# Optimization experiments

Hardware: AMD Instinct MI355X
Metric: run time of the kernel (lower is better)

## Reference

```python
import jax, jax.numpy as jnp
import numpy as np

# dims: N batch, C in-channels, T frames, V joints, H heads, HD per-head dim, O out-channels
N, C, T, V = 32, 64, 256, 25
H, HD, O = 8, 8, 64  # HD = max(C//8, 8)
SCALE = HD ** -0.5
EPS = 1e-5


def setup_inputs() -> dict:
    key = jax.random.key(0)
    ks = jax.random.split(key, 10)
    return {
        "x": jax.random.normal(ks[0], (N, C, T, V), jnp.float32),
        "ln_gamma": jnp.ones((C,), jnp.float32),
        "ln_beta": jnp.zeros((C,), jnp.float32),
        "w_qk": jax.random.normal(ks[1], (C, 2 * H * HD), jnp.float32),  # to_qk init N(0,1)
        "b_qk": jax.random.normal(ks[2], (2 * H * HD,), jnp.float32) * 0.02,
        "shared_topology": jax.random.uniform(ks[3], (H, V, V), jnp.float32),
        "conv_w": jax.random.normal(ks[4], (H, O, C), jnp.float32) * np.sqrt(2.0 / (O * H)),
        "conv_b": jnp.zeros((H, O), jnp.float32),
        "bn_gamma": jnp.full((O,), 1e-6, jnp.float32),
        "bn_beta": jnp.zeros((O,), jnp.float32),
        "bn_mean": jnp.zeros((O,), jnp.float32),
        "bn_var": jnp.ones((O,), jnp.float32),
    }


def reference(x, ln_gamma, ln_beta, w_qk, b_qk, shared_topology,
              conv_w, conv_b, bn_gamma, bn_beta, bn_mean, bn_var):
    # ---- SelfAttention over joints ----
    y = jnp.transpose(x, (0, 2, 3, 1))                 # [N,T,V,C]
    mu = jnp.mean(y, axis=-1, keepdims=True)
    var = jnp.var(y, axis=-1, keepdims=True)
    yn = (y - mu) * jax.lax.rsqrt(var + EPS) * ln_gamma + ln_beta
    qk = yn @ w_qk + b_qk                              # [N,T,V,2*H*HD]
    B = N * T
    q, k = jnp.split(qk.reshape(B, V, 2 * H * HD), 2, axis=-1)
    q = q.reshape(B, V, H, HD).transpose(0, 2, 1, 3)   # [B,H,V,HD]
    k = k.reshape(B, V, H, HD).transpose(0, 2, 1, 3)
    dots = jnp.einsum("bhid,bhjd->bhij", q, k) * SCALE
    attn = jax.nn.softmax(dots, axis=-1).astype(jnp.float32)  # [B,H,V,V]

    # ---- attention-gated graph conv ----
    A = attn * shared_topology[None]                   # [B,H,V,V]
    feat = jnp.transpose(x, (0, 2, 3, 1)).reshape(B, V, C)  # [B,V,C]
    z = jnp.einsum("bhuv,bvc->bhuc", A, feat)          # per-head aggregate [B,H,V,C]
    # fused per-head 1x1 convs + sum over heads
    out = jnp.einsum("bhuc,hoc->buo", z, conv_w) + conv_b.sum(0)  # [B,V,O]
    out = out.reshape(N, T, V, O).transpose(0, 3, 1, 2)           # [N,O,T,V]

    # ---- BatchNorm (inference-mode) + residual + ReLU ----
    g = (bn_gamma * jax.lax.rsqrt(bn_var + EPS))[None, :, None, None]
    b = (bn_beta - bn_mean * bn_gamma * jax.lax.rsqrt(bn_var + EPS))[None, :, None, None]
    out = out * g + b
    out = jax.nn.relu(out + x)  # down is identity (in_c == out_c)
    return out
```

## Files before the change

### kernel.cpp

```cpp
#include <hip/hip_runtime.h>
#include <math.h>

#define SCALE_L2E 0.51006972157f
#define EPSV 1e-5f

typedef __attribute__((ext_vector_type(8))) short bf16x8;
typedef __attribute__((ext_vector_type(4))) float f32x4;
typedef __attribute__((ext_vector_type(16))) float f32x16;
typedef __attribute__((ext_vector_type(4))) int i32x4;
typedef __attribute__((ext_vector_type(2))) int i32x2;

static __device__ __forceinline__ unsigned short bfh(float f) {
    return (unsigned short)(__builtin_bit_cast(unsigned int, f) >> 16);
}
static __device__ __forceinline__ int pack2(float lo, float hi) {
    return __builtin_amdgcn_perm(__builtin_bit_cast(unsigned int, hi),
                                 __builtin_bit_cast(unsigned int, lo), 0x07060302u);
}
#define LGKM0() __asm__ __volatile__("s_waitcnt lgkmcnt(0)" ::: "memory")

__global__ void prep_kernel(const float* __restrict__ w_qk,
                            const float* __restrict__ conv_w,
                            const float* __restrict__ conv_b,
                            const float* __restrict__ bn_g, const float* __restrict__ bn_b,
                            const float* __restrict__ bn_m, const float* __restrict__ bn_v,
                            unsigned short* __restrict__ ws) {
    int i = blockIdx.x * 256 + threadIdx.x;
    if (i < 8192) {
        int f = i >> 9, rem = i & 511, l = rem >> 3, j = rem & 7;
        int nt = f >> 1, ks = f & 1;
        int k = ks * 32 + (l >> 4) * 8 + j;
        int nn = nt * 16 + (l & 15);
        ws[i] = bfh(w_qk[k * 128 + nn]);
    } else if (i < 40960) {
        int i2 = i - 8192;
        int g = i2 >> 9, rem = i2 & 511, l = rem >> 3, j = rem & 7;
        int h = g >> 3, nt = (g >> 1) & 3, ks = g & 1;
        int c = ks * 32 + (l >> 4) * 8 + j;
        int o = nt * 16 + (l & 15);
        ws[i] = bfh(conv_w[h * 4096 + o * 64 + c]);
    } else if (i < 41024) {
        int o = i - 40960;
        float gv = bn_g[o] * rsqrtf(bn_v[o] + EPSV);
        float bb = bn_b[o] - bn_m[o] * gv;
        float cb = 0.f;
        for (int h = 0; h < 8; h++) cb += conv_b[h * 64 + o];
        float* wsf = (float*)(ws + 40960);
        wsf[o] = gv;
        wsf[64 + o] = bb + cb * gv;
    }
}

__global__ __launch_bounds__(256, 2)
void sagc_kernel(const float* __restrict__ x,
                 const float* __restrict__ ln_g, const float* __restrict__ ln_b,
                 const float* __restrict__ b_qk,
                 const float* __restrict__ topo,
                 const unsigned short* __restrict__ ws,
                 float* __restrict__ out)
{
    __shared__ __align__(16) unsigned char smem[36864];
    const int tid = threadIdx.x;
    const int lane = tid & 63, wv = tid >> 6;
    const int l15 = lane & 15, quad = lane >> 4;
    const int r32 = lane & 31, hi = lane >> 5;

    unsigned char* my = smem + wv * 9216;
    unsigned short* qbuf = (unsigned short*)my;
    unsigned short* kbuf = (unsigned short*)(my + 1536);
    unsigned char*  fwb  = my;
    unsigned char*  pb0  = my + 4096;
    unsigned char*  pb1  = my + 4096 + 2560;

    const unsigned short* wqk = ws;
    const unsigned short* w2f = ws + 8192;
    const float* bnA = (const float*)(ws + 40960);
    const float* bnB = bnA + 64;

    const int tile = blockIdx.x * 4 + wv;
    const int n = tile >> 8, t = tile & 255;
    const float* xg = x + (size_t)n * 409600 + (size_t)t * 25;
    float* og = out + (size_t)n * 409600 + (size_t)t * 25;

    float xf[2][2][8];
    #pragma unroll
    for (int mt = 0; mt < 2; mt++) {
        const int v = mt * 16 + l15;
        const bool ok = (v < 25);
        const float* xc = xg + v;
        #pragma unroll
        for (int ks = 0; ks < 2; ks++)
            #pragma unroll
            for (int j = 0; j < 8; j++) {
                int c = ks * 32 + quad * 8 + j;
                xf[mt][ks][j] = ok ? xc[c * 6400] : 0.f;
            }
    }

    bf16x8 xa[2][2];
    float sum_[2] = {0.f, 0.f}, ssq_[2] = {0.f, 0.f};
    #pragma unroll
    for (int mt = 0; mt < 2; mt++)
        #pragma unroll
        for (int ks = 0; ks < 2; ks++) {
            i32x4 pa;
            #pragma unroll
            for (int q = 0; q < 4; q++)
                pa[q] = pack2(xf[mt][ks][2 * q], xf[mt][ks][2 * q + 1]);
            xa[mt][ks] = __builtin_bit_cast(bf16x8, pa);
            #pragma unroll
            for (int j = 0; j < 8; j++) {
                float a = xf[mt][ks][j];
                sum_[mt] += a;
                ssq_[mt] += a * a;
            }
        }

    float muv[2], rsv[2];
    #pragma unroll
    for (int mt = 0; mt < 2; mt++) {
        sum_[mt] += __shfl_xor(sum_[mt], 16);
        sum_[mt] += __shfl_xor(sum_[mt], 32);
        ssq_[mt] += __shfl_xor(ssq_[mt], 16);
        ssq_[mt] += __shfl_xor(ssq_[mt], 32);
        muv[mt] = sum_[mt] * 0.015625f;
        rsv[mt] = rsqrtf(ssq_[mt] * 0.015625f - muv[mt] * muv[mt] + EPSV);
    }

    bf16x8 yna[2][2];
    #pragma unroll
    for (int ks = 0; ks < 2; ks++) {
        f32x4 ga = *(const f32x4*)&ln_g[ks * 32 + quad * 8];
        f32x4 gb = *(const f32x4*)&ln_g[ks * 32 + quad * 8 + 4];
        f32x4 ba = *(const f32x4*)&ln_b[ks * 32 + quad * 8];
        f32x4 bb = *(const f32x4*)&ln_b[ks * 32 + quad * 8 + 4];
        #pragma unroll
        for (int mt = 0; mt < 2; mt++) {
            float yv[8];
            #pragma unroll
            for (int j = 0; j < 8; j++) {
                float g = (j < 4) ? ga[j] : gb[j - 4];
                float bt = (j < 4) ? ba[j] : bb[j - 4];
                yv[j] = (xf[mt][ks][j] - muv[mt]) * rsv[mt] * g + bt;
            }
            i32x4 p;
            #pragma unroll
            for (int q = 0; q < 4; q++) p[q] = pack2(yv[2 * q], yv[2 * q + 1]);
            yna[mt][ks] = __builtin_bit_cast(bf16x8, p);
        }
    }

    f32x4 acc[2][4];
    #pragma unroll
    for (int mt = 0; mt < 2; mt++)
        #pragma unroll
        for (int nt = 0; nt < 4; nt++)
            acc[mt][nt] = (f32x4){0.f, 0.f, 0.f, 0.f};

    const f32x4 z4 = {0.f, 0.f, 0.f, 0.f};
    const bf16x8 z8 = {0, 0, 0, 0, 0, 0, 0, 0};

    const int sw4 = (l15 >> 2) & 3;
    unsigned char* w0p = fwb + ((((quad >> 1) ^ sw4)) << 4) + (quad & 1) * 8;
    unsigned char* w1p = fwb + (((((quad >> 1) ^ sw4)) ^ 2) << 4) + (quad & 1) * 8;
    unsigned char* brp = fwb + l15 * 64 + ((quad ^ sw4) << 4);

    const int uc = (r32 < 25) ? r32 : 24;

    auto softmax_store = [&](f32x16& dd, const float* tp, unsigned char* Pb) {
        dd[12] = hi ? -3e30f : dd[12];
        dd[13] = -3e30f; dd[14] = -3e30f; dd[15] = -3e30f;
        float t8[8];
        #pragma unroll
        for (int r = 0; r < 8; r++) t8[r] = fmaxf(dd[r], dd[r + 8]);
        #pragma unroll
        for (int r = 0; r < 4; r++) t8[r] = fmaxf(t8[r], t8[r + 4]);
        float m = fmaxf(fmaxf(t8[0], t8[1]), fmaxf(t8[2], t8[3]));
        m = fmaxf(m, __shfl_xor(m, 32));
        float s0 = 0.f, s1 = 0.f, s2 = 0.f, s3 = 0.f;
        #pragma unroll
        for (int r = 0; r < 16; r += 4) {
            dd[r]     = __builtin_amdgcn_exp2f(dd[r] - m);     s0 += dd[r];
            dd[r + 1] = __builtin_amdgcn_exp2f(dd[r + 1] - m); s1 += dd[r + 1];
            dd[r + 2] = __builtin_amdgcn_exp2f(dd[r + 2] - m); s2 += dd[r + 2];
            dd[r + 3] = __builtin_amdgcn_exp2f(dd[r + 3] - m); s3 += dd[r + 3];
        }
        float s = (s0 + s1) + (s2 + s3);
        s += __shfl_xor(s, 32);
        float inv = __builtin_amdgcn_rcpf(s);
        #pragma unroll
        for (int r = 0; r < 16; r++) dd[r] = dd[r] * inv * tp[r];
        if (r32 < 25) {
            unsigned char* rowp = Pb + r32 * 80 + hi * 8;
            *(i32x2*)(rowp +  0) = (i32x2){pack2(dd[0], dd[1]),   pack2(dd[2], dd[3])};
            *(i32x2*)(rowp + 16) = (i32x2){pack2(dd[4], dd[5]),   pack2(dd[6], dd[7])};
            *(i32x2*)(rowp + 32) = (i32x2){pack2(dd[8], dd[9]),   pack2(dd[10], dd[11])};
            *(i32x2*)(rowp + 48) = (i32x2){pack2(dd[12], dd[13]), pack2(dd[14], dd[15])};
        }
    };

    const f32x16 z16 = {0.f,0.f,0.f,0.f,0.f,0.f,0.f,0.f,0.f,0.f,0.f,0.f,0.f,0.f,0.f,0.f};

    #pragma unroll
    for (int hp = 0; hp < 4; hp++) {
        #pragma unroll
        for (int tsel = 0; tsel < 2; tsel++) {
            int nt = tsel ? (4 + hp) : hp;
            bf16x8 b0 = *(const bf16x8*)&wqk[(nt * 2 + 0) * 512 + lane * 8];
            bf16x8 b1 = *(const bf16x8*)&wqk[(nt * 2 + 1) * 512 + lane * 8];
            float bias = b_qk[(tsel ? 64 : 0) + hp * 16 + l15];
            unsigned short* buf = tsel ? kbuf : qbuf;
            #pragma unroll
            for (int mt = 0; mt < 2; mt++) {
                f32x4 d = __builtin_amdgcn_mfma_f32_16x16x32_bf16(yna[mt][0], b0, z4, 0, 0, 0);
                d = __builtin_amdgcn_mfma_f32_16x16x32_bf16(yna[mt][1], b1, d, 0, 0, 0);
                #pragma unroll
                for (int r = 0; r < 4; r++) {
                    int u = mt * 16 + quad * 4 + r;
                    if (u < 25) {
                        float val = d[r] + bias;
                        if (!tsel) val *= SCALE_L2E;
                        buf[u * 24 + l15] = bfh(val);
                    }
                }
            }
        }

        float tp0[16];
        {
            const float* tb = topo + (hp * 2 + 0) * 625 + uc * 25 + hi * 4;
            #pragma unroll
            for (int r = 0; r < 16; r++) {
                int off = (r < 12) ? ((r & 3) + (r >> 2) * 8)
                        : (r == 12 ? (hi ? 0 : 24) : 0);
                tp0[r] = tb[off];
            }
        }
        LGKM0();

        f32x16 p0;
        {
            bf16x8 ak = z8, bq = z8;
            if (hi == 0) {
                ak = *(const bf16x8*)&kbuf[r32 * 24 + 0];
                bq = *(const bf16x8*)&qbuf[r32 * 24 + 0];
            }
            p0 = __builtin_amdgcn_mfma_f32_32x32x16_bf16(ak, bq, z16, 0, 0, 0);
        }
        float tp1[16];
        {
            const float* tb = topo + (hp * 2 + 1) * 625 + uc * 25 + hi * 4;
            #pragma unroll
            for (int r = 0; r < 16; r++) {
                int off = (r < 12) ? ((r & 3) + (r >> 2) * 8)
                        : (r == 12 ? (hi ? 0 : 24) : 0);
                tp1[r] = tb[off];
            }
        }
        f32x16 p1;
        {
            bf16x8 ak = z8, bq = z8;
            if (hi == 0) {
                ak = *(const bf16x8*)&kbuf[r32 * 24 + 8];
                bq = *(const bf16x8*)&qbuf[r32 * 24 + 8];
            }
            p1 = __builtin_amdgcn_mfma_f32_32x32x16_bf16(ak, bq, z16, 0, 0, 0);
        }

        softmax_store(p0, tp0, pb0);
        softmax_store(p1, tp1, pb1);

        bf16x8 w2e[8];
        #pragma unroll
        for (int nt = 0; nt < 4; nt++) {
            int h = hp * 2;
            w2e[2 * nt]     = *(const bf16x8*)&w2f[((h * 4 + nt) * 2 + 0) * 512 + lane * 8];
            w2e[2 * nt + 1] = *(const bf16x8*)&w2f[((h * 4 + nt) * 2 + 1) * 512 + lane * 8];
        }

        #pragma unroll
        for (int nt = 0; nt < 4; nt++) {
            f32x4 dw0 = __builtin_amdgcn_mfma_f32_16x16x32_bf16(xa[0][0], w2e[2 * nt], z4, 0, 0, 0);
            dw0 = __builtin_amdgcn_mfma_f32_16x16x32_bf16(xa[0][1], w2e[2 * nt + 1], dw0, 0, 0, 0);
            f32x4 dw1 = __builtin_amdgcn_mfma_f32_16x16x32_bf16(xa[1][0], w2e[2 * nt], z4, 0, 0, 0);
            dw1 = __builtin_amdgcn_mfma_f32_16x16x32_bf16(xa[1][1], w2e[2 * nt + 1], dw1, 0, 0, 0);
            i32x2 q0 = {pack2(dw0[0], dw0[1]), pack2(dw0[2], dw0[3])};
            i32x2 q1 = {pack2(dw1[0], dw1[1]), pack2(dw1[2], dw1[3])};
            *(i32x2*)(w0p + nt * 1024 + l15 * 64) = q0;
            *(i32x2*)(w1p + nt * 1024 + l15 * 64) = q1;
        }
        bf16x8 w2o[8];
        #pragma unroll
        for (int nt = 0; nt < 4; nt++) {
            int h = hp * 2 + 1;
            w2o[2 * nt]     = *(const bf16x8*)&w2f[((h * 4 + nt) * 2 + 0) * 512 + lane * 8];
            w2o[2 * nt + 1] = *(const bf16x8*)&w2f[((h * 4 + nt) * 2 + 1) * 512 + lane * 8];
        }
        LGKM0();

        {
            bf16x8 ag0 = *(const bf16x8*)(pb0 + l15 * 80 + quad * 16);
            bf16x8 ag1 = *(const bf16x8*)(pb0 + (16 + l15) * 80 + quad * 16);
            #pragma unroll
            for (int nt = 0; nt < 4; nt++) {
                bf16x8 br = *(const bf16x8*)(brp + nt * 1024);
                acc[0][nt] = __builtin_amdgcn_mfma_f32_16x16x32_bf16(ag0, br, acc[0][nt], 0, 0, 0);
                acc[1][nt] = __builtin_amdgcn_mfma_f32_16x16x32_bf16(ag1, br, acc[1][nt], 0, 0, 0);
            }
        }

        #pragma unroll
        for (int nt = 0; nt < 4; nt++) {
            f32x4 dw0 = __builtin_amdgcn_mfma_f32_16x16x32_bf16(xa[0][0], w2o[2 * nt], z4, 0, 0, 0);
            dw0 = __builtin_amdgcn_mfma_f32_16x16x32_bf16(xa[0][1], w2o[2 * nt + 1], dw0, 0, 0, 0);
            f32x4 dw1 = __builtin_amdgcn_mfma_f32_16x16x32_bf16(xa[1][0], w2o[2 * nt], z4, 0, 0, 0);
            dw1 = __builtin_amdgcn_mfma_f32_16x16x32_bf16(xa[1][1], w2o[2 * nt + 1], dw1, 0, 0, 0);
            i32x2 q0 = {pack2(dw0[0], dw0[1]), pack2(dw0[2], dw0[3])};
            i32x2 q1 = {pack2(dw1[0], dw1[1]), pack2(dw1[2], dw1[3])};
            *(i32x2*)(w0p + nt * 1024 + l15 * 64) = q0;
            *(i32x2*)(w1p + nt * 1024 + l15 * 64) = q1;
        }
        LGKM0();

        {
            bf16x8 ag0 = *(const bf16x8*)(pb1 + l15 * 80 + quad * 16);
            bf16x8 ag1 = *(const bf16x8*)(pb1 + (16 + l15) * 80 + quad * 16);
            #pragma unroll
            for (int nt = 0; nt < 4; nt++) {
                bf16x8 br = *(const bf16x8*)(brp + nt * 1024);
                acc[0][nt] = __builtin_amdgcn_mfma_f32_16x16x32_bf16(ag0, br, acc[0][nt], 0, 0, 0);
                acc[1][nt] = __builtin_amdgcn_mfma_f32_16x16x32_bf16(ag1, br, acc[1][nt], 0, 0, 0);
            }
        }
    }

    #pragma unroll
    for (int nt = 0; nt < 4; nt++) {
        int o = nt * 16 + l15;
        float gA = bnA[o], gB = bnB[o];
        #pragma unroll
        for (int mt = 0; mt < 2; mt++) {
            int ub = mt * 16 + quad * 4;
            #pragma unroll
            for (int r = 0; r < 4; r++) {
                int u = ub + r;
                if (u < 25) {
                    float val = acc[mt][nt][r] * gA + gB + xg[o * 6400 + u];
                    og[o * 6400 + u] = fmaxf(val, 0.f);
                }
            }
        }
    }
}

extern "C" void kernel_launch(void* const* d_in, const int* in_sizes, int n_in,
                              void* d_out, int out_size, void* d_ws, size_t ws_size,
                              hipStream_t stream) {
    const float* x      = (const float*)d_in[0];
    const float* ln_g   = (const float*)d_in[1];
    const float* ln_b   = (const float*)d_in[2];
    const float* w_qk   = (const float*)d_in[3];
    const float* b_qk   = (const float*)d_in[4];
    const float* topo   = (const float*)d_in[5];
    const float* conv_w = (const float*)d_in[6];
    const float* conv_b = (const float*)d_in[7];
    const float* bn_g   = (const float*)d_in[8];
    const float* bn_b   = (const float*)d_in[9];
    const float* bn_m   = (const float*)d_in[10];
    const float* bn_v   = (const float*)d_in[11];
    float* outp = (float*)d_out;
    unsigned short* wsp = (unsigned short*)d_ws;

    hipLaunchKernelGGL(prep_kernel, dim3(161), dim3(256), 0, stream,
                       w_qk, conv_w, conv_b, bn_g, bn_b, bn_m, bn_v, wsp);
    hipLaunchKernelGGL(sagc_kernel, dim3(2048), dim3(256), 0, stream,
                       x, ln_g, ln_b, b_qk, topo, (const unsigned short*)wsp, outp);
}
```

Baseline: 188.8 us.

## Process two time-frame tiles per wavefront to reuse weight and topology loads

Each wave now handles two adjacent (n,t) tiles instead of one, with the grid halved and per-wave shared memory doubled. Weight fragments (w_qk, conv_w) and topology gathers are loaded once per head and used for both tiles, and the independent MFMA chains of the two tiles are interleaved to hide latency. In exchange, register pressure roughly doubles, launch bounds drop to one block per SIMD group, and LDS use doubles, which lowers occupancy.

```diff
diff --git a/kernel.cpp b/kernel.cpp
--- a/kernel.cpp
+++ b/kernel.cpp
@@ -18,6 +18,7 @@
                                  __builtin_bit_cast(unsigned int, lo), 0x07060302u);
 }
 #define LGKM0() __asm__ __volatile__("s_waitcnt lgkmcnt(0)" ::: "memory")
+#define MFMA16(a, b, c) __builtin_amdgcn_mfma_f32_16x16x32_bf16((a), (b), (c), 0, 0, 0)
 
 __global__ void prep_kernel(const float* __restrict__ w_qk,
                             const float* __restrict__ conv_w,
@@ -51,7 +52,7 @@
     }
 }
 
-__global__ __launch_bounds__(256, 2)
+__global__ __launch_bounds__(256, 1)
 void sagc_kernel(const float* __restrict__ x,
                  const float* __restrict__ ln_g, const float* __restrict__ ln_b,
                  const float* __restrict__ b_qk,
@@ -59,13 +60,13 @@
                  const unsigned short* __restrict__ ws,
                  float* __restrict__ out)
 {
-    __shared__ __align__(16) unsigned char smem[36864];
+    __shared__ __align__(16) unsigned char smem[73728];
     const int tid = threadIdx.x;
     const int lane = tid & 63, wv = tid >> 6;
     const int l15 = lane & 15, quad = lane >> 4;
     const int r32 = lane & 31, hi = lane >> 5;
 
-    unsigned char* my = smem + wv * 9216;
+    unsigned char* my = smem + wv * 18432;
     unsigned short* qbuf = (unsigned short*)my;
     unsigned short* kbuf = (unsigned short*)(my + 1536);
     unsigned char*  fwb  = my;
@@ -77,88 +78,94 @@
     const float* bnA = (const float*)(ws + 40960);
     const float* bnB = bnA + 64;
 
-    const int tile = blockIdx.x * 4 + wv;
-    const int n = tile >> 8, t = tile & 255;
-    const float* xg = x + (size_t)n * 409600 + (size_t)t * 25;
-    float* og = out + (size_t)n * 409600 + (size_t)t * 25;
-
-    float xf[2][2][8];
-    #pragma unroll
-    for (int mt = 0; mt < 2; mt++) {
-        const int v = mt * 16 + l15;
-        const bool ok = (v < 25);
-        const float* xc = xg + v;
-        #pragma unroll
-        for (int ks = 0; ks < 2; ks++)
-            #pragma unroll
-            for (int j = 0; j < 8; j++) {
-                int c = ks * 32 + quad * 8 + j;
-                xf[mt][ks][j] = ok ? xc[c * 6400] : 0.f;
+    const int tileA = (blockIdx.x * 4 + wv) * 2;
+    const int n = tileA >> 8, tA = tileA & 255;
+    const float* xgA = x + (size_t)n * 409600 + (size_t)tA * 25;
+    const float* xgB = xgA + 25;
+    float* ogA = out + (size_t)n * 409600 + (size_t)tA * 25;
+    float* ogB = ogA + 25;
+
+    auto prologue = [&](const float* xg, bf16x8 (&xa)[2][2], bf16x8 (&yna)[2][2]) {
+        float xf[2][2][8];
+        #pragma unroll
+        for (int mt = 0; mt < 2; mt++) {
+            const int v = mt * 16 + l15;
+            const bool ok = (v < 25);
+            const float* xc = xg + v;
+            #pragma unroll
+            for (int ks = 0; ks < 2; ks++)
+                #pragma unroll
+                for (int j = 0; j < 8; j++) {
+                    int c = ks * 32 + quad * 8 + j;
+                    xf[mt][ks][j] = ok ? xc[c * 6400] : 0.f;
+                }
+        }
+        float sum_[2] = {0.f, 0.f}, ssq_[2] = {0.f, 0.f};
+        #pragma unroll
+        for (int mt = 0; mt < 2; mt++)
+            #pragma unroll
+            for (int ks = 0; ks < 2; ks++) {
+                i32x4 pa;
+                #pragma unroll
+                for (int q = 0; q < 4; q++)
+                    pa[q] = pack2(xf[mt][ks][2 * q], xf[mt][ks][2 * q + 1]);
+                xa[mt][ks] = __builtin_bit_cast(bf16x8, pa);
+                #pragma unroll
+                for (int j = 0; j < 8; j++) {
+                    float a = xf[mt][ks][j];
+                    sum_[mt] += a;
+                    ssq_[mt] += a * a;
+                }
             }
-    }
-
-    bf16x8 xa[2][2];
-    float sum_[2] = {0.f, 0.f}, ssq_[2] = {0.f, 0.f};
+        float muv[2], rsv[2];
+        #pragma unroll
+        for (int mt = 0; mt < 2; mt++) {
+            sum_[mt] += __shfl_xor(sum_[mt], 16);
+            sum_[mt] += __shfl_xor(sum_[mt], 32);
+            ssq_[mt] += __shfl_xor(ssq_[mt], 16);
+            ssq_[mt] += __shfl_xor(ssq_[mt], 32);
+            muv[mt] = sum_[mt] * 0.015625f;
+            rsv[mt] = rsqrtf(ssq_[mt] * 0.015625f - muv[mt] * muv[mt] + EPSV);
+        }
+        #pragma unroll
+        for (int ks = 0; ks < 2; ks++) {
+            f32x4 ga = *(const f32x4*)&ln_g[ks * 32 + quad * 8];
+            f32x4 gb = *(const f32x4*)&ln_g[ks * 32 + quad * 8 + 4];
+            f32x4 ba = *(const f32x4*)&ln_b[ks * 32 + quad * 8];
+            f32x4 bb = *(const f32x4*)&ln_b[ks * 32 + quad * 8 + 4];
+            #pragma unroll
+            for (int mt = 0; mt < 2; mt++) {
+                float yv[8];
+                #pragma unroll
+                for (int j = 0; j < 8; j++) {
+                    float g = (j < 4) ? ga[j] : gb[j - 4];
+                    float bt = (j < 4) ? ba[j] : bb[j - 4];
+                    yv[j] = (xf[mt][ks][j] - muv[mt]) * rsv[mt] * g + bt;
+                }
+                i32x4 p;
+                #pragma unroll
+                for (int q = 0; q < 4; q++) p[q] = pack2(yv[2 * q], yv[2 * q + 1]);
+                yna[mt][ks] = __builtin_bit_cast(bf16x8, p);
+            }
+        }
+    };
+
+    bf16x8 xaA[2][2], ynaA[2][2], xaB[2][2], ynaB[2][2];
+    prologue(xgA, xaA, ynaA);
+    prologue(xgB, xaB, ynaB);
+
+    f32x4 accA[2][4], accB[2][4];
     #pragma unroll
     for (int mt = 0; mt < 2; mt++)
         #pragma unroll
-        for (int ks = 0; ks < 2; ks++) {
-            i32x4 pa;
-            #pragma unroll
-            for (int q = 0; q < 4; q++)
-                pa[q] = pack2(xf[mt][ks][2 * q], xf[mt][ks][2 * q + 1]);
-            xa[mt][ks] = __builtin_bit_cast(bf16x8, pa);
-            #pragma unroll
-            for (int j = 0; j < 8; j++) {
-                float a = xf[mt][ks][j];
-                sum_[mt] += a;
-                ssq_[mt] += a * a;
-            }
-        }
-
-    float muv[2], rsv[2];
-    #pragma unroll
-    for (int mt = 0; mt < 2; mt++) {
-        sum_[mt] += __shfl_xor(sum_[mt], 16);
-        sum_[mt] += __shfl_xor(sum_[mt], 32);
-        ssq_[mt] += __shfl_xor(ssq_[mt], 16);
-        ssq_[mt] += __shfl_xor(ssq_[mt], 32);
-        muv[mt] = sum_[mt] * 0.015625f;
-        rsv[mt] = rsqrtf(ssq_[mt] * 0.015625f - muv[mt] * muv[mt] + EPSV);
-    }
-
-    bf16x8 yna[2][2];
-    #pragma unroll
-    for (int ks = 0; ks < 2; ks++) {
-        f32x4 ga = *(const f32x4*)&ln_g[ks * 32 + quad * 8];
-        f32x4 gb = *(const f32x4*)&ln_g[ks * 32 + quad * 8 + 4];
-        f32x4 ba = *(const f32x4*)&ln_b[ks * 32 + quad * 8];
-        f32x4 bb = *(const f32x4*)&ln_b[ks * 32 + quad * 8 + 4];
-        #pragma unroll
-        for (int mt = 0; mt < 2; mt++) {
-            float yv[8];
-            #pragma unroll
-            for (int j = 0; j < 8; j++) {
-                float g = (j < 4) ? ga[j] : gb[j - 4];
-                float bt = (j < 4) ? ba[j] : bb[j - 4];
-                yv[j] = (xf[mt][ks][j] - muv[mt]) * rsv[mt] * g + bt;
-            }
-            i32x4 p;
-            #pragma unroll
-            for (int q = 0; q < 4; q++) p[q] = pack2(yv[2 * q], yv[2 * q + 1]);
-            yna[mt][ks] = __builtin_bit_cast(bf16x8, p);
-        }
-    }
-
-    f32x4 acc[2][4];
-    #pragma unroll
-    for (int mt = 0; mt < 2; mt++)
-        #pragma unroll
-        for (int nt = 0; nt < 4; nt++)
-            acc[mt][nt] = (f32x4){0.f, 0.f, 0.f, 0.f};
+        for (int nt = 0; nt < 4; nt++) {
+            accA[mt][nt] = (f32x4){0.f, 0.f, 0.f, 0.f};
+            accB[mt][nt] = (f32x4){0.f, 0.f, 0.f, 0.f};
+        }
 
     const f32x4 z4 = {0.f, 0.f, 0.f, 0.f};
     const bf16x8 z8 = {0, 0, 0, 0, 0, 0, 0, 0};
+    const f32x16 z16 = {0.f,0.f,0.f,0.f,0.f,0.f,0.f,0.f,0.f,0.f,0.f,0.f,0.f,0.f,0.f,0.f};
 
     const int sw4 = (l15 >> 2) & 3;
     unsigned char* w0p = fwb + ((((quad >> 1) ^ sw4)) << 4) + (quad & 1) * 8;
@@ -199,9 +206,50 @@
         }
     };
 
-    const f32x16 z16 = {0.f,0.f,0.f,0.f,0.f,0.f,0.f,0.f,0.f,0.f,0.f,0.f,0.f,0.f,0.f,0.f};
-
-    #pragma unroll
+    auto topo_gather = [&](int h, float (&tp)[16]) {
+        const float* tb = topo + h * 625 + uc * 25 + hi * 4;
+        #pragma unroll
+        for (int r = 0; r < 16; r++) {
+            int off = (r < 12) ? ((r & 3) + (r >> 2) * 8)
+                    : (r == 12 ? (hi ? 0 : 24) : 0);
+            tp[r] = tb[off];
+        }
+    };
+
+    auto dots = [&](int tdoff, int hh) -> f32x16 {
+        bf16x8 ak = z8, bq = z8;
+        if (hi == 0) {
+            ak = *(const bf16x8*)((unsigned char*)kbuf + tdoff + r32 * 48 + hh * 16);
+            bq = *(const bf16x8*)((unsigned char*)qbuf + tdoff + r32 * 48 + hh * 16);
+        }
+        return __builtin_amdgcn_mfma_f32_32x32x16_bf16(ak, bq, z16, 0, 0, 0);
+    };
+
+    auto fw_phase = [&](bf16x8 (&xa)[2][2], const bf16x8* w2, int tdoff) {
+        #pragma unroll
+        for (int nt = 0; nt < 4; nt++) {
+            f32x4 dw0 = MFMA16(xa[0][0], w2[2 * nt], z4);
+            dw0 = MFMA16(xa[0][1], w2[2 * nt + 1], dw0);
+            f32x4 dw1 = MFMA16(xa[1][0], w2[2 * nt], z4);
+            dw1 = MFMA16(xa[1][1], w2[2 * nt + 1], dw1);
+            i32x2 q0 = {pack2(dw0[0], dw0[1]), pack2(dw0[2], dw0[3])};
+            i32x2 q1 = {pack2(dw1[0], dw1[1]), pack2(dw1[2], dw1[3])};
+            *(i32x2*)(w0p + tdoff + nt * 1024 + l15 * 64) = q0;
+            *(i32x2*)(w1p + tdoff + nt * 1024 + l15 * 64) = q1;
+        }
+    };
+
+    auto pv_phase = [&](f32x4 (&acc)[2][4], unsigned char* Pb, int tdoff) {
+        bf16x8 ag0 = *(const bf16x8*)(Pb + tdoff + l15 * 80 + quad * 16);
+        bf16x8 ag1 = *(const bf16x8*)(Pb + tdoff + 1280 + l15 * 80 + quad * 16);
+        #pragma unroll
+        for (int nt = 0; nt < 4; nt++) {
+            bf16x8 br = *(const bf16x8*)(brp + tdoff + nt * 1024);
+            acc[0][nt] = MFMA16(ag0, br, acc[0][nt]);
+            acc[1][nt] = MFMA16(ag1, br, acc[1][nt]);
+        }
+    };
+
     for (int hp = 0; hp < 4; hp++) {
         #pragma unroll
         for (int tsel = 0; tsel < 2; tsel++) {
@@ -209,66 +257,45 @@
             bf16x8 b0 = *(const bf16x8*)&wqk[(nt * 2 + 0) * 512 + lane * 8];
             bf16x8 b1 = *(const bf16x8*)&wqk[(nt * 2 + 1) * 512 + lane * 8];
             float bias = b_qk[(tsel ? 64 : 0) + hp * 16 + l15];
-            unsigned short* buf = tsel ? kbuf : qbuf;
-            #pragma unroll
-            for (int mt = 0; mt < 2; mt++) {
-                f32x4 d = __builtin_amdgcn_mfma_f32_16x16x32_bf16(yna[mt][0], b0, z4, 0, 0, 0);
-                d = __builtin_amdgcn_mfma_f32_16x16x32_bf16(yna[mt][1], b1, d, 0, 0, 0);
-                #pragma unroll
-                for (int r = 0; r < 4; r++) {
-                    int u = mt * 16 + quad * 4 + r;
-                    if (u < 25) {
-                        float val = d[r] + bias;
-                        if (!tsel) val *= SCALE_L2E;
-                        buf[u * 24 + l15] = bfh(val);
+            #pragma unroll
+            for (int td = 0; td < 2; td++) {
+                unsigned short* buf = (unsigned short*)((unsigned char*)(tsel ? kbuf : qbuf) + td * 9216);
+                #pragma unroll
+                for (int mt = 0; mt < 2; mt++) {
+                    const bf16x8* yn = td ? ynaB[mt] : ynaA[mt];
+                    f32x4 d = MFMA16(yn[0], b0, z4);
+                    d = MFMA16(yn[1], b1, d);
+                    #pragma unroll
+                    for (int r = 0; r < 4; r++) {
+                        int u = mt * 16 + quad * 4 + r;
+                        if (u < 25) {
+                            float val = d[r] + bias;
+                            if (!tsel) val *= SCALE_L2E;
+                            buf[u * 24 + l15] = bfh(val);
+                        }
                     }
                 }
             }
         }
 
         float tp0[16];
+        topo_gather(hp * 2, tp0);
+        LGKM0();
+
         {
-            const float* tb = topo + (hp * 2 + 0) * 625 + uc * 25 + hi * 4;
-            #pragma unroll
-            for (int r = 0; r < 16; r++) {
-                int off = (r < 12) ? ((r & 3) + (r >> 2) * 8)
-                        : (r == 12 ? (hi ? 0 : 24) : 0);
-                tp0[r] = tb[off];
-            }
-        }
-        LGKM0();
-
-        f32x16 p0;
+            f32x16 pA = dots(0, 0);
+            f32x16 pB = dots(9216, 0);
+            softmax_store(pA, tp0, pb0);
+            softmax_store(pB, tp0, pb0 + 9216);
+        }
+        float tp1[16];
+        topo_gather(hp * 2 + 1, tp1);
         {
-            bf16x8 ak = z8, bq = z8;
-            if (hi == 0) {
-                ak = *(const bf16x8*)&kbuf[r32 * 24 + 0];
-                bq = *(const bf16x8*)&qbuf[r32 * 24 + 0];
-            }
-            p0 = __builtin_amdgcn_mfma_f32_32x32x16_bf16(ak, bq, z16, 0, 0, 0);
-        }
-        float tp1[16];
-        {
-            const float* tb = topo + (hp * 2 + 1) * 625 + uc * 25 + hi * 4;
-            #pragma unroll
-            for (int r = 0; r < 16; r++) {
-                int off = (r < 12) ? ((r & 3) + (r >> 2) * 8)
-                        : (r == 12 ? (hi ? 0 : 24) : 0);
-                tp1[r] = tb[off];
-            }
-        }
-        f32x16 p1;
-        {
-            bf16x8 ak = z8, bq = z8;
-            if (hi == 0) {
-                ak = *(const bf16x8*)&kbuf[r32 * 24 + 8];
-                bq = *(const bf16x8*)&qbuf[r32 * 24 + 8];
-            }
-            p1 = __builtin_amdgcn_mfma_f32_32x32x16_bf16(ak, bq, z16, 0, 0, 0);
-        }
-
-        softmax_store(p0, tp0, pb0);
-        softmax_store(p1, tp1, pb1);
+            f32x16 pA = dots(0, 1);
+            f32x16 pB = dots(9216, 1);
+            softmax_store(pA, tp1, pb1);
+            softmax_store(pB, tp1, pb1 + 9216);
+        }
 
         bf16x8 w2e[8];
         #pragma unroll
@@ -277,18 +304,8 @@
             w2e[2 * nt]     = *(const bf16x8*)&w2f[((h * 4 + nt) * 2 + 0) * 512 + lane * 8];
             w2e[2 * nt + 1] = *(const bf16x8*)&w2f[((h * 4 + nt) * 2 + 1) * 512 + lane * 8];
         }
-
-        #pragma unroll
-        for (int nt = 0; nt < 4; nt++) {
-            f32x4 dw0 = __builtin_amdgcn_mfma_f32_16x16x32_bf16(xa[0][0], w2e[2 * nt], z4, 0, 0, 0);
-            dw0 = __builtin_amdgcn_mfma_f32_16x16x32_bf16(xa[0][1], w2e[2 * nt + 1], dw0, 0, 0, 0);
-            f32x4 dw1 = __builtin_amdgcn_mfma_f32_16x16x32_bf16(xa[1][0], w2e[2 * nt], z4, 0, 0, 0);
-            dw1 = __builtin_amdgcn_mfma_f32_16x16x32_bf16(xa[1][1], w2e[2 * nt + 1], dw1, 0, 0, 0);
-            i32x2 q0 = {pack2(dw0[0], dw0[1]), pack2(dw0[2], dw0[3])};
-            i32x2 q1 = {pack2(dw1[0], dw1[1]), pack2(dw1[2], dw1[3])};
-            *(i32x2*)(w0p + nt * 1024 + l15 * 64) = q0;
-            *(i32x2*)(w1p + nt * 1024 + l15 * 64) = q1;
-        }
+        fw_phase(xaA, w2e, 0);
+        fw_phase(xaB, w2e, 9216);
         bf16x8 w2o[8];
         #pragma unroll
         for (int nt = 0; nt < 4; nt++) {
@@ -298,59 +315,38 @@
         }
         LGKM0();
 
-        {
-            bf16x8 ag0 = *(const bf16x8*)(pb0 + l15 * 80 + quad * 16);
-            bf16x8 ag1 = *(const bf16x8*)(pb0 + (16 + l15) * 80 + quad * 16);
-            #pragma unroll
-            for (int nt = 0; nt < 4; nt++) {
-                bf16x8 br = *(const bf16x8*)(brp + nt * 1024);
-                acc[0][nt] = __builtin_amdgcn_mfma_f32_16x16x32_bf16(ag0, br, acc[0][nt], 0, 0, 0);
-                acc[1][nt] = __builtin_amdgcn_mfma_f32_16x16x32_bf16(ag1, br, acc[1][nt], 0, 0, 0);
+        pv_phase(accA, pb0, 0);
+        pv_phase(accB, pb0, 9216);
+
+        fw_phase(xaA, w2o, 0);
+        fw_phase(xaB, w2o, 9216);
+        LGKM0();
+
+        pv_phase(accA, pb1, 0);
+        pv_phase(accB, pb1, 9216);
+    }
+
+    auto epilogue = [&](f32x4 (&acc)[2][4], const float* xg, float* og) {
+        #pragma unroll
+        for (int nt = 0; nt < 4; nt++) {
+            int o = nt * 16 + l15;
+            float gA = bnA[o], gB = bnB[o];
+            #pragma unroll
+            for (int mt = 0; mt < 2; mt++) {
+                int ub = mt * 16 + quad * 4;
+                #pragma unroll
+                for (int r = 0; r < 4; r++) {
+                    int u = ub + r;
+                    if (u < 25) {
+                        float val = acc[mt][nt][r] * gA + gB + xg[o * 6400 + u];
+                        og[o * 6400 + u] = fmaxf(val, 0.f);
+                    }
+                }
             }
         }
-
-        #pragma unroll
-        for (int nt = 0; nt < 4; nt++) {
-            f32x4 dw0 = __builtin_amdgcn_mfma_f32_16x16x32_bf16(xa[0][0], w2o[2 * nt], z4, 0, 0, 0);
-            dw0 = __builtin_amdgcn_mfma_f32_16x16x32_bf16(xa[0][1], w2o[2 * nt + 1], dw0, 0, 0, 0);
-            f32x4 dw1 = __builtin_amdgcn_mfma_f32_16x16x32_bf16(xa[1][0], w2o[2 * nt], z4, 0, 0, 0);
-            dw1 = __builtin_amdgcn_mfma_f32_16x16x32_bf16(xa[1][1], w2o[2 * nt + 1], dw1, 0, 0, 0);
-            i32x2 q0 = {pack2(dw0[0], dw0[1]), pack2(dw0[2], dw0[3])};
-            i32x2 q1 = {pack2(dw1[0], dw1[1]), pack2(dw1[2], dw1[3])};
-            *(i32x2*)(w0p + nt * 1024 + l15 * 64) = q0;
-            *(i32x2*)(w1p + nt * 1024 + l15 * 64) = q1;
-        }
-        LGKM0();
-
-        {
-            bf16x8 ag0 = *(const bf16x8*)(pb1 + l15 * 80 + quad * 16);
-            bf16x8 ag1 = *(const bf16x8*)(pb1 + (16 + l15) * 80 + quad * 16);
-            #pragma unroll
-            for (int nt = 0; nt < 4; nt++) {
-                bf16x8 br = *(const bf16x8*)(brp + nt * 1024);
-                acc[0][nt] = __builtin_amdgcn_mfma_f32_16x16x32_bf16(ag0, br, acc[0][nt], 0, 0, 0);
-                acc[1][nt] = __builtin_amdgcn_mfma_f32_16x16x32_bf16(ag1, br, acc[1][nt], 0, 0, 0);
-            }
-        }
-    }
-
-    #pragma unroll
-    for (int nt = 0; nt < 4; nt++) {
-        int o = nt * 16 + l15;
-        float gA = bnA[o], gB = bnB[o];
-        #pragma unroll
-        for (int mt = 0; mt < 2; mt++) {
-            int ub = mt * 16 + quad * 4;
-            #pragma unroll
-            for (int r = 0; r < 4; r++) {
-                int u = ub + r;
-                if (u < 25) {
-                    float val = acc[mt][nt][r] * gA + gB + xg[o * 6400 + u];
-                    og[o * 6400 + u] = fmaxf(val, 0.f);
-                }
-            }
-        }
-    }
+    };
+    epilogue(accA, xgA, ogA);
+    epilogue(accB, xgB, ogB);
 }
 
 extern "C" void kernel_launch(void* const* d_in, const int* in_sizes, int n_in,
@@ -373,6 +369,6 @@
 
     hipLaunchKernelGGL(prep_kernel, dim3(161), dim3(256), 0, stream,
                        w_qk, conv_w, conv_b, bn_g, bn_b, bn_m, bn_v, wsp);
-    hipLaunchKernelGGL(sagc_kernel, dim3(2048), dim3(256), 0, stream,
+    hipLaunchKernelGGL(sagc_kernel, dim3(1024), dim3(256), 0, stream,
                        x, ln_g, ln_b, b_qk, topo, (const unsigned short*)wsp, outp);
 }
```

Measured after the change: 220.4 us. +16.8%, slower.

## Split heads across wavefronts per tile with shared-memory cross-wave reduction

Applied to the files above, without the earlier changes.

Each block now handles one (n,t) tile, and each of its four wavefronts computes two of the eight heads instead of looping over all eight. The partial outputs are reduced across wavefronts through shared memory. The epilogue then writes vectorized float4 rows with one output channel per lane group. This gives four times as many blocks and a shorter serial per-wave chain, which should expose more parallelism. The cost is that every wave redundantly loads x and redoes layernorm, and the reduction adds two barriers and extra shared-memory traffic.

```diff
diff --git a/kernel.cpp b/kernel.cpp
--- a/kernel.cpp
+++ b/kernel.cpp
@@ -18,6 +18,7 @@
                                  __builtin_bit_cast(unsigned int, lo), 0x07060302u);
 }
 #define LGKM0() __asm__ __volatile__("s_waitcnt lgkmcnt(0)" ::: "memory")
+#define MFMA16(a, b, c) __builtin_amdgcn_mfma_f32_16x16x32_bf16((a), (b), (c), 0, 0, 0)
 
 __global__ void prep_kernel(const float* __restrict__ w_qk,
                             const float* __restrict__ conv_w,
@@ -70,17 +71,19 @@
     unsigned short* kbuf = (unsigned short*)(my + 1536);
     unsigned char*  fwb  = my;
     unsigned char*  pb0  = my + 4096;
-    unsigned char*  pb1  = my + 4096 + 2560;
+    unsigned char*  pb1  = my + 6656;
 
     const unsigned short* wqk = ws;
     const unsigned short* w2f = ws + 8192;
     const float* bnA = (const float*)(ws + 40960);
     const float* bnB = bnA + 64;
 
-    const int tile = blockIdx.x * 4 + wv;
+    const int tile = blockIdx.x;
     const int n = tile >> 8, t = tile & 255;
     const float* xg = x + (size_t)n * 409600 + (size_t)t * 25;
     float* og = out + (size_t)n * 409600 + (size_t)t * 25;
+
+    const int hp = wv;
 
     float xf[2][2][8];
     #pragma unroll
@@ -96,7 +99,6 @@
                 xf[mt][ks][j] = ok ? xc[c * 6400] : 0.f;
             }
     }
-
     bf16x8 xa[2][2];
     float sum_[2] = {0.f, 0.f}, ssq_[2] = {0.f, 0.f};
     #pragma unroll
@@ -115,7 +117,6 @@
                 ssq_[mt] += a * a;
             }
         }
-
     float muv[2], rsv[2];
     #pragma unroll
     for (int mt = 0; mt < 2; mt++) {
@@ -126,7 +127,6 @@
         muv[mt] = sum_[mt] * 0.015625f;
         rsv[mt] = rsqrtf(ssq_[mt] * 0.015625f - muv[mt] * muv[mt] + EPSV);
     }
-
     bf16x8 yna[2][2];
     #pragma unroll
     for (int ks = 0; ks < 2; ks++) {
@@ -159,6 +159,7 @@
 
     const f32x4 z4 = {0.f, 0.f, 0.f, 0.f};
     const bf16x8 z8 = {0, 0, 0, 0, 0, 0, 0, 0};
+    const f32x16 z16 = {0.f,0.f,0.f,0.f,0.f,0.f,0.f,0.f,0.f,0.f,0.f,0.f,0.f,0.f,0.f,0.f};
 
     const int sw4 = (l15 >> 2) & 3;
     unsigned char* w0p = fwb + ((((quad >> 1) ^ sw4)) << 4) + (quad & 1) * 8;
@@ -199,155 +200,159 @@
         }
     };
 
-    const f32x16 z16 = {0.f,0.f,0.f,0.f,0.f,0.f,0.f,0.f,0.f,0.f,0.f,0.f,0.f,0.f,0.f,0.f};
-
-    #pragma unroll
-    for (int hp = 0; hp < 4; hp++) {
-        #pragma unroll
-        for (int tsel = 0; tsel < 2; tsel++) {
-            int nt = tsel ? (4 + hp) : hp;
-            bf16x8 b0 = *(const bf16x8*)&wqk[(nt * 2 + 0) * 512 + lane * 8];
-            bf16x8 b1 = *(const bf16x8*)&wqk[(nt * 2 + 1) * 512 + lane * 8];
-            float bias = b_qk[(tsel ? 64 : 0) + hp * 16 + l15];
-            unsigned short* buf = tsel ? kbuf : qbuf;
-            #pragma unroll
-            for (int mt = 0; mt < 2; mt++) {
-                f32x4 d = __builtin_amdgcn_mfma_f32_16x16x32_bf16(yna[mt][0], b0, z4, 0, 0, 0);
-                d = __builtin_amdgcn_mfma_f32_16x16x32_bf16(yna[mt][1], b1, d, 0, 0, 0);
+    auto topo_gather = [&](int h, float (&tp)[16]) {
+        const float* tb = topo + h * 625 + uc * 25 + hi * 4;
+        #pragma unroll
+        for (int r = 0; r < 16; r++) {
+            int off = (r < 12) ? ((r & 3) + (r >> 2) * 8)
+                    : (r == 12 ? (hi ? 0 : 24) : 0);
+            tp[r] = tb[off];
+        }
+    };
+
+    #pragma unroll
+    for (int tsel = 0; tsel < 2; tsel++) {
+        int nt = tsel ? (4 + hp) : hp;
+        bf16x8 b0 = *(const bf16x8*)&wqk[(nt * 2 + 0) * 512 + lane * 8];
+        bf16x8 b1 = *(const bf16x8*)&wqk[(nt * 2 + 1) * 512 + lane * 8];
+        float bias = b_qk[(tsel ? 64 : 0) + hp * 16 + l15];
+        unsigned short* buf = tsel ? kbuf : qbuf;
+        #pragma unroll
+        for (int mt = 0; mt < 2; mt++) {
+            f32x4 d = MFMA16(yna[mt][0], b0, z4);
+            d = MFMA16(yna[mt][1], b1, d);
+            #pragma unroll
+            for (int r = 0; r < 4; r++) {
+                int u = mt * 16 + quad * 4 + r;
+                if (u < 25) {
+                    float val = d[r] + bias;
+                    if (!tsel) val *= SCALE_L2E;
+                    buf[u * 24 + l15] = bfh(val);
+                }
+            }
+        }
+    }
+
+    float tp0[16];
+    topo_gather(hp * 2, tp0);
+    LGKM0();
+
+    f32x16 p0, p1;
+    {
+        bf16x8 ak = z8, bq = z8;
+        if (hi == 0) {
+            ak = *(const bf16x8*)&kbuf[r32 * 24 + 0];
+            bq = *(const bf16x8*)&qbuf[r32 * 24 + 0];
+        }
+        p0 = __builtin_amdgcn_mfma_f32_32x32x16_bf16(ak, bq, z16, 0, 0, 0);
+    }
+    float tp1[16];
+    topo_gather(hp * 2 + 1, tp1);
+    {
+        bf16x8 ak = z8, bq = z8;
+        if (hi == 0) {
+            ak = *(const bf16x8*)&kbuf[r32 * 24 + 8];
+            bq = *(const bf16x8*)&qbuf[r32 * 24 + 8];
+        }
+        p1 = __builtin_amdgcn_mfma_f32_32x32x16_bf16(ak, bq, z16, 0, 0, 0);
+    }
+    softmax_store(p0, tp0, pb0);
+    softmax_store(p1, tp1, pb1);
+
+    bf16x8 w2e[8];
+    #pragma unroll
+    for (int nt = 0; nt < 4; nt++) {
+        int h = hp * 2;
+        w2e[2 * nt]     = *(const bf16x8*)&w2f[((h * 4 + nt) * 2 + 0) * 512 + lane * 8];
+        w2e[2 * nt + 1] = *(const bf16x8*)&w2f[((h * 4 + nt) * 2 + 1) * 512 + lane * 8];
+    }
+    #pragma unroll
+    for (int nt = 0; nt < 4; nt++) {
+        f32x4 dw0 = MFMA16(xa[0][0], w2e[2 * nt], z4);
+        dw0 = MFMA16(xa[0][1], w2e[2 * nt + 1], dw0);
+        f32x4 dw1 = MFMA16(xa[1][0], w2e[2 * nt], z4);
+        dw1 = MFMA16(xa[1][1], w2e[2 * nt + 1], dw1);
+        i32x2 q0 = {pack2(dw0[0], dw0[1]), pack2(dw0[2], dw0[3])};
+        i32x2 q1 = {pack2(dw1[0], dw1[1]), pack2(dw1[2], dw1[3])};
+        *(i32x2*)(w0p + nt * 1024 + l15 * 64) = q0;
+        *(i32x2*)(w1p + nt * 1024 + l15 * 64) = q1;
+    }
+    bf16x8 w2o[8];
+    #pragma unroll
+    for (int nt = 0; nt < 4; nt++) {
+        int h = hp * 2 + 1;
+        w2o[2 * nt]     = *(const bf16x8*)&w2f[((h * 4 + nt) * 2 + 0) * 512 + lane * 8];
+        w2o[2 * nt + 1] = *(const bf16x8*)&w2f[((h * 4 + nt) * 2 + 1) * 512 + lane * 8];
+    }
+    LGKM0();
+
+    {
+        bf16x8 ag0 = *(const bf16x8*)(pb0 + l15 * 80 + quad * 16);
+        bf16x8 ag1 = *(const bf16x8*)(pb0 + 1280 + l15 * 80 + quad * 16);
+        #pragma unroll
+        for (int nt = 0; nt < 4; nt++) {
+            bf16x8 br = *(const bf16x8*)(brp + nt * 1024);
+            acc[0][nt] = MFMA16(ag0, br, acc[0][nt]);
+            acc[1][nt] = MFMA16(ag1, br, acc[1][nt]);
+        }
+    }
+
+    #pragma unroll
+    for (int nt = 0; nt < 4; nt++) {
+        f32x4 dw0 = MFMA16(xa[0][0], w2o[2 * nt], z4);
+        dw0 = MFMA16(xa[0][1], w2o[2 * nt + 1], dw0);
+        f32x4 dw1 = MFMA16(xa[1][0], w2o[2 * nt], z4);
+        dw1 = MFMA16(xa[1][1], w2o[2 * nt + 1], dw1);
+        i32x2 q0 = {pack2(dw0[0], dw0[1]), pack2(dw0[2], dw0[3])};
+        i32x2 q1 = {pack2(dw1[0], dw1[1]), pack2(dw1[2], dw1[3])};
+        *(i32x2*)(w0p + nt * 1024 + l15 * 64) = q0;
+        *(i32x2*)(w1p + nt * 1024 + l15 * 64) = q1;
+    }
+    LGKM0();
+
+    {
+        bf16x8 ag0 = *(const bf16x8*)(pb1 + l15 * 80 + quad * 16);
+        bf16x8 ag1 = *(const bf16x8*)(pb1 + 1280 + l15 * 80 + quad * 16);
+        #pragma unroll
+        for (int nt = 0; nt < 4; nt++) {
+            bf16x8 br = *(const bf16x8*)(brp + nt * 1024);
+            acc[0][nt] = MFMA16(ag0, br, acc[0][nt]);
+            acc[1][nt] = MFMA16(ag1, br, acc[1][nt]);
+        }
+    }
+
+    __syncthreads();
+    {
+        float* red = (float*)smem + wv * 2304;
+        #pragma unroll
+        for (int mt = 0; mt < 2; mt++)
+            #pragma unroll
+            for (int nt = 0; nt < 4; nt++)
+                *(f32x4*)&red[(nt * 16 + l15) * 36 + mt * 16 + quad * 4] = acc[mt][nt];
+    }
+    __syncthreads();
+
+    {
+        const float* redf = (const float*)smem;
+        const int o = wv * 16 + l15;
+        const float gA = bnA[o], gB = bnB[o];
+        const float* xo = xg + (size_t)o * 6400;
+        float* oo = og + (size_t)o * 6400;
+        #pragma unroll
+        for (int mt = 0; mt < 2; mt++) {
+            const int ub = mt * 16 + quad * 4;
+            f32x4 s = {0.f, 0.f, 0.f, 0.f};
+            #pragma unroll
+            for (int w = 0; w < 4; w++)
+                s += *(const f32x4*)&redf[w * 2304 + o * 36 + ub];
+            if (ub + 3 < 25) {
+                f32x4 xr = *(const f32x4*)&xo[ub];
+                f32x4 v;
                 #pragma unroll
-                for (int r = 0; r < 4; r++) {
-                    int u = mt * 16 + quad * 4 + r;
-                    if (u < 25) {
-                        float val = d[r] + bias;
-                        if (!tsel) val *= SCALE_L2E;
-                        buf[u * 24 + l15] = bfh(val);
-                    }
-                }
-            }
-        }
-
-        float tp0[16];
-        {
-            const float* tb = topo + (hp * 2 + 0) * 625 + uc * 25 + hi * 4;
-            #pragma unroll
-            for (int r = 0; r < 16; r++) {
-                int off = (r < 12) ? ((r & 3) + (r >> 2) * 8)
-                        : (r == 12 ? (hi ? 0 : 24) : 0);
-                tp0[r] = tb[off];
-            }
-        }
-        LGKM0();
-
-        f32x16 p0;
-        {
-            bf16x8 ak = z8, bq = z8;
-            if (hi == 0) {
-                ak = *(const bf16x8*)&kbuf[r32 * 24 + 0];
-                bq = *(const bf16x8*)&qbuf[r32 * 24 + 0];
-            }
-            p0 = __builtin_amdgcn_mfma_f32_32x32x16_bf16(ak, bq, z16, 0, 0, 0);
-        }
-        float tp1[16];
-        {
-            const float* tb = topo + (hp * 2 + 1) * 625 + uc * 25 + hi * 4;
-            #pragma unroll
-            for (int r = 0; r < 16; r++) {
-                int off = (r < 12) ? ((r & 3) + (r >> 2) * 8)
-                        : (r == 12 ? (hi ? 0 : 24) : 0);
-                tp1[r] = tb[off];
-            }
-        }
-        f32x16 p1;
-        {
-            bf16x8 ak = z8, bq = z8;
-            if (hi == 0) {
-                ak = *(const bf16x8*)&kbuf[r32 * 24 + 8];
-                bq = *(const bf16x8*)&qbuf[r32 * 24 + 8];
-            }
-            p1 = __builtin_amdgcn_mfma_f32_32x32x16_bf16(ak, bq, z16, 0, 0, 0);
-        }
-
-        softmax_store(p0, tp0, pb0);
-        softmax_store(p1, tp1, pb1);
-
-        bf16x8 w2e[8];
-        #pragma unroll
-        for (int nt = 0; nt < 4; nt++) {
-            int h = hp * 2;
-            w2e[2 * nt]     = *(const bf16x8*)&w2f[((h * 4 + nt) * 2 + 0) * 512 + lane * 8];
-            w2e[2 * nt + 1] = *(const bf16x8*)&w2f[((h * 4 + nt) * 2 + 1) * 512 + lane * 8];
-        }
-
-        #pragma unroll
-        for (int nt = 0; nt < 4; nt++) {
-            f32x4 dw0 = __builtin_amdgcn_mfma_f32_16x16x32_bf16(xa[0][0], w2e[2 * nt], z4, 0, 0, 0);
-            dw0 = __builtin_amdgcn_mfma_f32_16x16x32_bf16(xa[0][1], w2e[2 * nt + 1], dw0, 0, 0, 0);
-            f32x4 dw1 = __builtin_amdgcn_mfma_f32_16x16x32_bf16(xa[1][0], w2e[2 * nt], z4, 0, 0, 0);
-            dw1 = __builtin_amdgcn_mfma_f32_16x16x32_bf16(xa[1][1], w2e[2 * nt + 1], dw1, 0, 0, 0);
-            i32x2 q0 = {pack2(dw0[0], dw0[1]), pack2(dw0[2], dw0[3])};
-            i32x2 q1 = {pack2(dw1[0], dw1[1]), pack2(dw1[2], dw1[3])};
-            *(i32x2*)(w0p + nt * 1024 + l15 * 64) = q0;
-            *(i32x2*)(w1p + nt * 1024 + l15 * 64) = q1;
-        }
-        bf16x8 w2o[8];
-        #pragma unroll
-        for (int nt = 0; nt < 4; nt++) {
-            int h = hp * 2 + 1;
-            w2o[2 * nt]     = *(const bf16x8*)&w2f[((h * 4 + nt) * 2 + 0) * 512 + lane * 8];
-            w2o[2 * nt + 1] = *(const bf16x8*)&w2f[((h * 4 + nt) * 2 + 1) * 512 + lane * 8];
-        }
-        LGKM0();
-
-        {
-            bf16x8 ag0 = *(const bf16x8*)(pb0 + l15 * 80 + quad * 16);
-            bf16x8 ag1 = *(const bf16x8*)(pb0 + (16 + l15) * 80 + quad * 16);
-            #pragma unroll
-            for (int nt = 0; nt < 4; nt++) {
-                bf16x8 br = *(const bf16x8*)(brp + nt * 1024);
-                acc[0][nt] = __builtin_amdgcn_mfma_f32_16x16x32_bf16(ag0, br, acc[0][nt], 0, 0, 0);
-                acc[1][nt] = __builtin_amdgcn_mfma_f32_16x16x32_bf16(ag1, br, acc[1][nt], 0, 0, 0);
-            }
-        }
-
-        #pragma unroll
-        for (int nt = 0; nt < 4; nt++) {
-            f32x4 dw0 = __builtin_amdgcn_mfma_f32_16x16x32_bf16(xa[0][0], w2o[2 * nt], z4, 0, 0, 0);
-            dw0 = __builtin_amdgcn_mfma_f32_16x16x32_bf16(xa[0][1], w2o[2 * nt + 1], dw0, 0, 0, 0);
-            f32x4 dw1 = __builtin_amdgcn_mfma_f32_16x16x32_bf16(xa[1][0], w2o[2 * nt], z4, 0, 0, 0);
-            dw1 = __builtin_amdgcn_mfma_f32_16x16x32_bf16(xa[1][1], w2o[2 * nt + 1], dw1, 0, 0, 0);
-            i32x2 q0 = {pack2(dw0[0], dw0[1]), pack2(dw0[2], dw0[3])};
-            i32x2 q1 = {pack2(dw1[0], dw1[1]), pack2(dw1[2], dw1[3])};
-            *(i32x2*)(w0p + nt * 1024 + l15 * 64) = q0;
-            *(i32x2*)(w1p + nt * 1024 + l15 * 64) = q1;
-        }
-        LGKM0();
-
-        {
-            bf16x8 ag0 = *(const bf16x8*)(pb1 + l15 * 80 + quad * 16);
-            bf16x8 ag1 = *(const bf16x8*)(pb1 + (16 + l15) * 80 + quad * 16);
-            #pragma unroll
-            for (int nt = 0; nt < 4; nt++) {
-                bf16x8 br = *(const bf16x8*)(brp + nt * 1024);
-                acc[0][nt] = __builtin_amdgcn_mfma_f32_16x16x32_bf16(ag0, br, acc[0][nt], 0, 0, 0);
-                acc[1][nt] = __builtin_amdgcn_mfma_f32_16x16x32_bf16(ag1, br, acc[1][nt], 0, 0, 0);
-            }
-        }
-    }
-
-    #pragma unroll
-    for (int nt = 0; nt < 4; nt++) {
-        int o = nt * 16 + l15;
-        float gA = bnA[o], gB = bnB[o];
-        #pragma unroll
-        for (int mt = 0; mt < 2; mt++) {
-            int ub = mt * 16 + quad * 4;
-            #pragma unroll
-            for (int r = 0; r < 4; r++) {
-                int u = ub + r;
-                if (u < 25) {
-                    float val = acc[mt][nt][r] * gA + gB + xg[o * 6400 + u];
-                    og[o * 6400 + u] = fmaxf(val, 0.f);
-                }
+                for (int r = 0; r < 4; r++) v[r] = fmaxf(s[r] * gA + gB + xr[r], 0.f);
+                *(f32x4*)&oo[ub] = v;
+            } else if (ub < 25) {
+                oo[ub] = fmaxf(s[0] * gA + gB + xo[ub], 0.f);
             }
         }
     }
@@ -373,6 +378,6 @@
 
     hipLaunchKernelGGL(prep_kernel, dim3(161), dim3(256), 0, stream,
                        w_qk, conv_w, conv_b, bn_g, bn_b, bn_m, bn_v, wsp);
-    hipLaunchKernelGGL(sagc_kernel, dim3(2048), dim3(256), 0, stream,
+    hipLaunchKernelGGL(sagc_kernel, dim3(8192), dim3(256), 0, stream,
                        x, ln_g, ln_b, b_qk, topo, (const unsigned short*)wsp, outp);
 }
```

Result: slower. 193.5 us (+2.5%).
